# Kernel optimization log

Hardware: AMD Instinct MI355X
Metric: run time of the kernel (lower is better)

Reference implementation:

```python
import jax, jax.numpy as jnp
import numpy as np
import math

B, L, D, H = 2, 2048, 1024, 16
DK = D // H  # 64


def _lin(k, din, dout):
    kw, kb = jax.random.split(k)
    w = jax.random.normal(kw, (din, dout), dtype=jnp.float32) * 0.02
    b = jax.random.normal(kb, (dout,), dtype=jnp.float32) * 0.02
    return w, b


def setup_inputs() -> dict:
    key = jax.random.key(0)
    ks = jax.random.split(key, 12)
    wq, bq = _lin(ks[0], D, D)
    wk, bk = _lin(ks[1], D, D)
    wv, bv = _lin(ks[2], D, D)
    wo, bo = _lin(ks[3], D, D)
    whq, bhq = _lin(ks[4], DK, DK)
    whk, bhk = _lin(ks[5], DK, DK)
    whv, bhv = _lin(ks[6], DK, DK)
    who, bho = _lin(ks[7], DK, DK)
    return {
        "q_input": jax.random.normal(ks[8], (B, L, D), dtype=jnp.float32),
        "k_input": jax.random.normal(ks[9], (B, L, D), dtype=jnp.float32),
        "v_input": jax.random.normal(ks[10], (B, L, D), dtype=jnp.float32),
        "mask": jnp.ones((B, 1, L, L), dtype=jnp.int32),
        "wq": wq, "bq": bq, "wk": wk, "bk": bk, "wv": wv, "bv": bv,
        "wo": wo, "bo": bo,
        "whq": whq, "bhq": bhq, "whk": whk, "bhk": bhk,
        "whv": whv, "bhv": bhv, "who": who, "bho": bho,
    }


def reference(q_input, k_input, v_input, mask, wq, bq, wk, bk, wv, bv, wo, bo,
              whq, bhq, whk, bhk, whv, bhv, who, bho):
    scale = 1.0 / math.sqrt(DK)
    # Q/K/V projections -> [B, H, L, DK]
    Q = (q_input @ wq + bq).reshape(B, L, H, DK).transpose(0, 2, 1, 3)
    K = (k_input @ wk + bk).reshape(B, L, H, DK).transpose(0, 2, 1, 3)
    V = (v_input @ wv + bv).reshape(B, L, H, DK).transpose(0, 2, 1, 3)
    scores = jnp.einsum('bhqd,bhkd->bhqk', Q, K) * scale  # [B,H,L,L]
    neg = jnp.finfo(scores.dtype).min
    scores = jnp.where(mask == 0, neg, scores)
    probs = jax.nn.softmax(scores, axis=-1)  # dropout is identity in eval
    attn = jnp.einsum('bhqk,bhkd->bhqd', probs, V)
    heads = attn.transpose(0, 2, 1, 3)  # [B, L, H, DK]
    # Inter-head attention over the head dimension (size H) per position
    Qh = heads @ whq + bhq
    Kh = heads @ whk + bhk
    Vh = heads @ whv + bhv
    inter = jnp.einsum('blhd,blgd->blhg', Qh, Kh) * scale  # [B,L,H,H]
    iprobs = jax.nn.softmax(inter, axis=-1)
    mixed = jnp.einsum('blhg,blgd->blhd', iprobs, Vh)  # [B,L,H,DK]
    # note: inter_head_out is defined but unused in the original forward
    concat = mixed.reshape(B, L, D)
    return concat @ wo + bo
```

## Files before the change

### kernel.cpp

```cpp
#include <hip/hip_runtime.h>
#include <hip/hip_bf16.h>

typedef __bf16 bf16_t;
typedef __bf16 bf16x4 __attribute__((ext_vector_type(4)));
typedef __bf16 bf16x8 __attribute__((ext_vector_type(8)));
typedef float f32x4 __attribute__((ext_vector_type(4)));

typedef __attribute__((address_space(1))) unsigned char glob_u8;
typedef __attribute__((address_space(3))) unsigned char lds_u8;

__device__ __forceinline__ void load_lds16(const void* g, void* l) {
    __builtin_amdgcn_global_load_lds((glob_u8*)g, (lds_u8*)l, 16, 0, 0);
}

__global__ void prep1_kernel(const int* __restrict__ mask, int* __restrict__ flags,
                             const float* __restrict__ wq, const float* __restrict__ wk,
                             const float* __restrict__ wv, bf16_t* __restrict__ wqkvT)
{
    const int bid = blockIdx.x, t = threadIdx.x;
    if (bid < 2048) {
        int b = bid >> 10, qt = (bid >> 5) & 31, kt = bid & 31;
        int ok = 1;
#pragma unroll
        for (int i = 0; i < 16; i++) {
            int e = t + i * 256; int r = e >> 6, c = e & 63;
            ok &= (mask[((size_t)b * 2048 + qt * 64 + r) * 2048 + kt * 64 + c] != 0) ? 1 : 0;
        }
        ok = __syncthreads_and(ok);
        if (t == 0) flags[bid] = ok;
    } else {
        __shared__ bf16_t tile[64][65];
        int idx = bid - 2048;
        int z = idx >> 8, rem = idx & 255;
        const float* src = (z == 0) ? wq : (z == 1) ? wk : wv;
        bf16_t* dst = wqkvT + (size_t)z * 1048576;
        int rB = (rem >> 4) * 64, cB = (rem & 15) * 64;
#pragma unroll
        for (int i = 0; i < 16; i++) {
            int e = t + i * 256; int r = e >> 6, c = e & 63;
            tile[r][c] = (bf16_t)src[(size_t)(rB + r) * 1024 + cB + c];
        }
        __syncthreads();
#pragma unroll
        for (int i = 0; i < 16; i++) {
            int e = t + i * 256; int r = e >> 6, c = e & 63;
            dst[(size_t)(cB + r) * 1024 + rB + c] = tile[c][r];
        }
    }
}

__global__ void prep2_kernel(const float* __restrict__ wo, bf16_t* __restrict__ woT,
                             const float* __restrict__ s0, const float* __restrict__ s1,
                             const float* __restrict__ s2,
                             bf16_t* __restrict__ d0, bf16_t* __restrict__ d1, bf16_t* __restrict__ d2)
{
    const int bid = blockIdx.x, t = threadIdx.x;
    if (bid < 256) {
        __shared__ bf16_t tile[64][65];
        int rB = (bid >> 4) * 64, cB = (bid & 15) * 64;
#pragma unroll
        for (int i = 0; i < 16; i++) {
            int e = t + i * 256; int r = e >> 6, c = e & 63;
            tile[r][c] = (bf16_t)wo[(size_t)(rB + r) * 1024 + cB + c];
        }
        __syncthreads();
#pragma unroll
        for (int i = 0; i < 16; i++) {
            int e = t + i * 256; int r = e >> 6, c = e & 63;
            woT[(size_t)(cB + r) * 1024 + rB + c] = tile[c][r];
        }
    } else {
        int z = bid - 256;
        const float* src = (z == 0) ? s0 : (z == 1) ? s1 : s2;
        bf16_t* dst = (z == 0) ? d0 : (z == 1) ? d1 : d2;
#pragma unroll
        for (int i = 0; i < 16; i++) {
            int e = t + i * 256; int r = e >> 6, c = e & 63;
            dst[c * 64 + r] = (bf16_t)src[r * 64 + c];
        }
    }
}

__global__ __launch_bounds__(256, 2) void gemm_qkv_kernel(
    const float* __restrict__ Aq, const float* __restrict__ Ak, const float* __restrict__ Av,
    const bf16_t* __restrict__ WT,
    const float* __restrict__ bq, const float* __restrict__ bk, const float* __restrict__ bv,
    bf16_t* __restrict__ outbase)
{
    __shared__ float  Asf[2][128 * 32];
    __shared__ bf16_t Bs[2][128 * 32];
    const int z = blockIdx.z;
    const float* A    = (z == 0) ? Aq : (z == 1) ? Ak : Av;
    const bf16_t* Bt  = WT + (size_t)z * 1048576;
    const float* bia  = (z == 0) ? bq : (z == 1) ? bk : bv;
    bf16_t* out = outbase + (size_t)z * 4194304;

    const int t = threadIdx.x;
    const int w = t >> 6, lane = t & 63;
    const int lane15 = lane & 15, quad = lane >> 4;
    const int wr = w >> 1, wc = w & 1;
    const int rowBase = blockIdx.x * 128, colBase = blockIdx.y * 128;

    const int arow = lane >> 3;
    const int achk = (lane & 7) ^ arow;
    const int brow = lane >> 2;
    const int bchk = (lane & 3) ^ ((brow >> 1) & 3);

    const float*  aspA[4];
#pragma unroll
    for (int d = 0; d < 4; d++)
        aspA[d] = A + (size_t)(rowBase + w * 32 + d * 8 + arow) * 1024 + achk * 4;
    const bf16_t* aspB[2];
#pragma unroll
    for (int d = 0; d < 2; d++)
        aspB[d] = Bt + (size_t)(colBase + w * 32 + d * 16 + brow) * 1024 + bchk * 8;

    f32x4 acc[4][4];
    f32x4 zf = {0.f, 0.f, 0.f, 0.f};
#pragma unroll
    for (int i = 0; i < 4; i++)
#pragma unroll
        for (int j = 0; j < 4; j++) acc[i][j] = zf;

    const int m7 = lane15 & 7;
    const int m3b = (lane15 >> 1) & 3;

#pragma unroll
    for (int d = 0; d < 4; d++)
        load_lds16(aspA[d], (char*)Asf[0] + (w * 32 + d * 8) * 128);
#pragma unroll
    for (int d = 0; d < 2; d++)
        load_lds16(aspB[d], (char*)Bs[0] + (w * 32 + d * 16) * 64);
    __syncthreads();

    for (int kt = 0; kt < 32; kt++) {
        const int cur = kt & 1, nxt = cur ^ 1;
        if (kt < 31) {
            const int k0 = (kt + 1) * 32;
#pragma unroll
            for (int d = 0; d < 4; d++)
                load_lds16(aspA[d] + k0, (char*)Asf[nxt] + (w * 32 + d * 8) * 128);
#pragma unroll
            for (int d = 0; d < 2; d++)
                load_lds16(aspB[d] + k0, (char*)Bs[nxt] + (w * 32 + d * 16) * 64);
        }

        bf16x8 afr[4], bfr[4];
#pragma unroll
        for (int mi = 0; mi < 4; mi++) {
            int row = wr * 64 + mi * 16 + lane15;
            int p0 = (quad * 2) ^ m7, p1 = (quad * 2 + 1) ^ m7;
            f32x4 u = *(const f32x4*)(Asf[cur] + row * 32 + p0 * 4);
            f32x4 v = *(const f32x4*)(Asf[cur] + row * 32 + p1 * 4);
            bf16x8 af;
            af[0] = (bf16_t)u[0]; af[1] = (bf16_t)u[1];
            af[2] = (bf16_t)u[2]; af[3] = (bf16_t)u[3];
            af[4] = (bf16_t)v[0]; af[5] = (bf16_t)v[1];
            af[6] = (bf16_t)v[2]; af[7] = (bf16_t)v[3];
            afr[mi] = af;
        }
#pragma unroll
        for (int ni = 0; ni < 4; ni++) {
            int row = wc * 64 + ni * 16 + lane15;
            int p = quad ^ m3b;
            bfr[ni] = *(const bf16x8*)(Bs[cur] + row * 32 + p * 8);
        }
#pragma unroll
        for (int mi = 0; mi < 4; mi++)
#pragma unroll
            for (int ni = 0; ni < 4; ni++)
                acc[mi][ni] = __builtin_amdgcn_mfma_f32_16x16x32_bf16(afr[mi], bfr[ni], acc[mi][ni], 0, 0, 0);

        __syncthreads();
    }

#pragma unroll
    for (int ni = 0; ni < 4; ni++) {
        int col = colBase + wc * 64 + ni * 16 + lane15;
        float bias = bia[col];
        int h = col >> 6, dk = col & 63;
#pragma unroll
        for (int mi = 0; mi < 4; mi++) {
#pragma unroll
            for (int r = 0; r < 4; r++) {
                int row = rowBase + wr * 64 + mi * 16 + quad * 4 + r;
                int b = row >> 11, l = row & 2047;
                float v = acc[mi][ni][r] + bias;
                size_t dst = (z < 2) ? ((((size_t)(b * 16 + h)) * 2048 + l) * 64 + dk)
                                     : ((((size_t)(b * 16 + h)) * 64 + dk) * 2048 + l);
                out[dst] = (bf16_t)v;
            }
        }
    }
}

__global__ __launch_bounds__(256, 2) void gemm_out_kernel(
    const bf16_t* __restrict__ A, const bf16_t* __restrict__ Bt,
    const float* __restrict__ bia, float* __restrict__ out)
{
    __shared__ bf16_t As[128 * 32];
    __shared__ bf16_t Bs[64 * 32];
    const int t = threadIdx.x;
    const int w = t >> 6, lane = t & 63;
    const int lane15 = lane & 15, quad = lane >> 4;
    const int wr = w >> 1, wc = w & 1;
    const int rowBase = blockIdx.x * 128, colBase = blockIdx.y * 64;

    const int brow = lane >> 2, bcol = (lane & 3) * 8;

    f32x4 acc[4][2];
    f32x4 zf = {0.f, 0.f, 0.f, 0.f};
#pragma unroll
    for (int i = 0; i < 4; i++)
#pragma unroll
        for (int j = 0; j < 2; j++) acc[i][j] = zf;

    for (int k0 = 0; k0 < 1024; k0 += 32) {
#pragma unroll
        for (int j = 0; j < 2; j++) {
            int chunk = w * 2 + j;
            load_lds16(A + (size_t)(rowBase + chunk * 16 + brow) * 1024 + k0 + bcol,
                       (char*)As + chunk * 1024);
        }
        {
            int chunk = w;
            load_lds16(Bt + (size_t)(colBase + chunk * 16 + brow) * 1024 + k0 + bcol,
                       (char*)Bs + chunk * 1024);
        }
        __syncthreads();
        bf16x8 afr[4], bfr[2];
#pragma unroll
        for (int mi = 0; mi < 4; mi++)
            afr[mi] = *(const bf16x8*)(As + (wr * 64 + mi * 16 + lane15) * 32 + quad * 8);
#pragma unroll
        for (int ni = 0; ni < 2; ni++)
            bfr[ni] = *(const bf16x8*)(Bs + (wc * 32 + ni * 16 + lane15) * 32 + quad * 8);
#pragma unroll
        for (int mi = 0; mi < 4; mi++)
#pragma unroll
            for (int ni = 0; ni < 2; ni++)
                acc[mi][ni] = __builtin_amdgcn_mfma_f32_16x16x32_bf16(afr[mi], bfr[ni], acc[mi][ni], 0, 0, 0);
        __syncthreads();
    }

#pragma unroll
    for (int ni = 0; ni < 2; ni++) {
        int col = colBase + wc * 32 + ni * 16 + lane15;
        float bias = bia[col];
#pragma unroll
        for (int mi = 0; mi < 4; mi++) {
#pragma unroll
            for (int r = 0; r < 4; r++) {
                int row = rowBase + wr * 64 + mi * 16 + quad * 4 + r;
                out[(size_t)row * 1024 + col] = acc[mi][ni][r] + bias;
            }
        }
    }
}

#define FS 72

__global__ __launch_bounds__(256, 2) void flash_kernel(
    const bf16_t* __restrict__ QKV, const int* __restrict__ mask,
    const int* __restrict__ flags, bf16_t* __restrict__ attnout)
{
    __shared__ bf16_t Ks[2][64 * FS];
    __shared__ bf16_t Vs[2][64 * FS];
    __shared__ bf16_t Ps[8 * 16 * FS];
    const int t = threadIdx.x, w = t >> 6, lane = t & 63;
    const int lane15 = lane & 15, quad = lane >> 4;
    const int qt = blockIdx.y, bh = blockIdx.x;
    const int b = bh >> 4, h = bh & 15;
    const bf16_t* Q  = QKV;
    const bf16_t* K  = QKV + 4194304;
    const bf16_t* Vt = QKV + 8388608;
    const int qrow0 = qt * 128 + w * 32;

    bf16x8 aq[2][2];
#pragma unroll
    for (int qf = 0; qf < 2; qf++) {
        const bf16_t* qb = Q + ((size_t)bh * 2048 + qrow0 + qf * 16 + lane15) * 64;
        aq[qf][0] = *(const bf16x8*)(qb + quad * 8);
        aq[qf][1] = *(const bf16x8*)(qb + 32 + quad * 8);
#pragma unroll
        for (int j = 0; j < 8; j++) {
            aq[qf][0][j] = (bf16_t)((float)aq[qf][0][j] * 0.125f);
            aq[qf][1][j] = (bf16_t)((float)aq[qf][1][j] * 0.125f);
        }
    }

    f32x4 zf = {0.f, 0.f, 0.f, 0.f};
    f32x4 o[2][4];
#pragma unroll
    for (int qf = 0; qf < 2; qf++)
#pragma unroll
        for (int df = 0; df < 4; df++) o[qf][df] = zf;
    f32x4 lsum[2] = {zf, zf};
    bf16_t* Pw0 = Ps + (w * 2 + 0) * 16 * FS;
    bf16_t* Pw1 = Ps + (w * 2 + 1) * 16 * FS;
    bf16x8 ones;
#pragma unroll
    for (int j = 0; j < 8; j++) ones[j] = (bf16_t)1.0f;

    const int e0 = t * 8, e1 = (256 + t) * 8;
    const int kr0 = e0 >> 6, kc0 = e0 & 63, kr1 = e1 >> 6, kc1 = e1 & 63;
    const int* flagrow = flags + (b * 32 + qt) * 32;
    const bf16_t* Kb  = K  + (size_t)bh * 131072;
    const bf16_t* Vtb = Vt + (size_t)bh * 131072;

    {
        bf16x8 k0v = *(const bf16x8*)(Kb  + (size_t)kr0 * 64 + kc0);
        bf16x8 k1v = *(const bf16x8*)(Kb  + (size_t)kr1 * 64 + kc1);
        bf16x8 v0v = *(const bf16x8*)(Vtb + (size_t)kr0 * 2048 + kc0);
        bf16x8 v1v = *(const bf16x8*)(Vtb + (size_t)kr1 * 2048 + kc1);
        *(bf16x8*)(Ks[0] + kr0 * FS + kc0) = k0v;
        *(bf16x8*)(Ks[0] + kr1 * FS + kc1) = k1v;
        *(bf16x8*)(Vs[0] + kr0 * FS + kc0) = v0v;
        *(bf16x8*)(Vs[0] + kr1 * FS + kc1) = v1v;
    }
    __syncthreads();

    for (int kt = 0; kt < 32; kt++) {
        const int cur = kt & 1, nxt = cur ^ 1;
        bf16x8 k0v, k1v, v0v, v1v;
        if (kt + 1 < 32) {
            int kn = (kt + 1) * 64;
            k0v = *(const bf16x8*)(Kb  + (size_t)(kn + kr0) * 64 + kc0);
            k1v = *(const bf16x8*)(Kb  + (size_t)(kn + kr1) * 64 + kc1);
            v0v = *(const bf16x8*)(Vtb + (size_t)kr0 * 2048 + kn + kc0);
            v1v = *(const bf16x8*)(Vtb + (size_t)kr1 * 2048 + kn + kc1);
        }

        f32x4 st[2][4];
#pragma unroll
        for (int kf = 0; kf < 4; kf++) {
            bf16x8 kb0 = *(const bf16x8*)(Ks[cur] + (kf * 16 + lane15) * FS + quad * 8);
            bf16x8 kb1 = *(const bf16x8*)(Ks[cur] + (kf * 16 + lane15) * FS + 32 + quad * 8);
#pragma unroll
            for (int qf = 0; qf < 2; qf++) {
                f32x4 a = zf;
                a = __builtin_amdgcn_mfma_f32_16x16x32_bf16(kb0, aq[qf][0], a, 0, 0, 0);
                a = __builtin_amdgcn_mfma_f32_16x16x32_bf16(kb1, aq[qf][1], a, 0, 0, 0);
                st[qf][kf] = a * 1.44269504f;
            }
        }
        if (kt + 1 < 32) {
            *(bf16x8*)(Ks[nxt] + kr0 * FS + kc0) = k0v;
            *(bf16x8*)(Ks[nxt] + kr1 * FS + kc1) = k1v;
            *(bf16x8*)(Vs[nxt] + kr0 * FS + kc0) = v0v;
            *(bf16x8*)(Vs[nxt] + kr1 * FS + kc1) = v1v;
        }
        if (!flagrow[kt]) {
#pragma unroll
            for (int qf = 0; qf < 2; qf++)
#pragma unroll
                for (int kf = 0; kf < 4; kf++)
#pragma unroll
                    for (int r = 0; r < 4; r++) {
                        int qrow = qrow0 + qf * 16 + lane15;
                        int kpos = kt * 64 + kf * 16 + quad * 4 + r;
                        if (mask[((size_t)b * 2048 + qrow) * 2048 + kpos] == 0)
                            st[qf][kf][r] = -1e30f;
                    }
        }
#pragma unroll
        for (int qf = 0; qf < 2; qf++) {
            bf16_t* Pq = qf ? Pw1 : Pw0;
#pragma unroll
            for (int kf = 0; kf < 4; kf++) {
                bf16x4 pv;
#pragma unroll
                for (int r = 0; r < 4; r++) pv[r] = (bf16_t)exp2f(st[qf][kf][r]);
                *(bf16x4*)(Pq + lane15 * FS + kf * 16 + quad * 4) = pv;
            }
        }
        bf16x8 pa[2][2];
        pa[0][0] = *(const bf16x8*)(Pw0 + lane15 * FS + quad * 8);
        pa[0][1] = *(const bf16x8*)(Pw0 + lane15 * FS + 32 + quad * 8);
        pa[1][0] = *(const bf16x8*)(Pw1 + lane15 * FS + quad * 8);
        pa[1][1] = *(const bf16x8*)(Pw1 + lane15 * FS + 32 + quad * 8);
#pragma unroll
        for (int qf = 0; qf < 2; qf++) {
            lsum[qf] = __builtin_amdgcn_mfma_f32_16x16x32_bf16(ones, pa[qf][0], lsum[qf], 0, 0, 0);
            lsum[qf] = __builtin_amdgcn_mfma_f32_16x16x32_bf16(ones, pa[qf][1], lsum[qf], 0, 0, 0);
        }
#pragma unroll
        for (int df = 0; df < 4; df++) {
            bf16x8 vb0 = *(const bf16x8*)(Vs[cur] + (df * 16 + lane15) * FS + quad * 8);
            bf16x8 vb1 = *(const bf16x8*)(Vs[cur] + (df * 16 + lane15) * FS + 32 + quad * 8);
#pragma unroll
            for (int qf = 0; qf < 2; qf++) {
                o[qf][df] = __builtin_amdgcn_mfma_f32_16x16x32_bf16(pa[qf][0], vb0, o[qf][df], 0, 0, 0);
                o[qf][df] = __builtin_amdgcn_mfma_f32_16x16x32_bf16(pa[qf][1], vb1, o[qf][df], 0, 0, 0);
            }
        }
        __syncthreads();
    }

#pragma unroll
    for (int qf = 0; qf < 2; qf++) {
        float lv = lsum[qf][0];
#pragma unroll
        for (int r = 0; r < 4; r++) {
            float inv = 1.0f / __shfl(lv, quad * 4 + r, 64);
            size_t row = (size_t)b * 2048 + qrow0 + qf * 16 + quad * 4 + r;
#pragma unroll
            for (int df = 0; df < 4; df++)
                attnout[(row * 16 + h) * 64 + df * 16 + lane15] = (bf16_t)(o[qf][df][r] * inv);
        }
    }
}

__global__ __launch_bounds__(256, 2) void interhead_kernel(
    const bf16_t* __restrict__ attn,
    const bf16_t* __restrict__ whqT, const float* __restrict__ bhq,
    const bf16_t* __restrict__ whkT, const float* __restrict__ bhk,
    const bf16_t* __restrict__ whvT, const float* __restrict__ bhv,
    bf16_t* __restrict__ concat)
{
    __shared__ bf16_t lds[4 * 4608];
    const int t = threadIdx.x, w = t >> 6, lane = t & 63;
    const int lane15 = lane & 15, quad = lane >> 4;
    bf16_t* Qh  = lds + w * 4608;
    bf16_t* Kh  = Qh + 1024;
    bf16_t* VhT = Kh + 1024;
    bf16_t* P16 = VhT + 2048;
    const int p = blockIdx.x * 4 + w;

    bf16x8 z8 = {(bf16_t)0.f, (bf16_t)0.f, (bf16_t)0.f, (bf16_t)0.f,
                 (bf16_t)0.f, (bf16_t)0.f, (bf16_t)0.f, (bf16_t)0.f};
    ((bf16x8*)P16)[lane] = z8;
#pragma unroll
    for (int i = 0; i < 4; i++) ((bf16x8*)VhT)[i * 64 + lane] = z8;

    const bf16_t* hb = attn + ((size_t)p * 16 + lane15) * 64;
    bf16x8 ha0 = *(const bf16x8*)(hb + quad * 8);
    bf16x8 ha1 = *(const bf16x8*)(hb + 32 + quad * 8);

    const bf16_t* Wt[3] = {whqT, whkT, whvT};
    const float*  Bb[3] = {bhq, bhk, bhv};
    f32x4 zf = {0.f, 0.f, 0.f, 0.f};
#pragma unroll
    for (int m3 = 0; m3 < 3; m3++) {
#pragma unroll
        for (int nf = 0; nf < 4; nf++) {
            f32x4 acc = zf;
            bf16x8 wb0 = *(const bf16x8*)(Wt[m3] + (nf * 16 + lane15) * 64 + quad * 8);
            bf16x8 wb1 = *(const bf16x8*)(Wt[m3] + (nf * 16 + lane15) * 64 + 32 + quad * 8);
            acc = __builtin_amdgcn_mfma_f32_16x16x32_bf16(ha0, wb0, acc, 0, 0, 0);
            acc = __builtin_amdgcn_mfma_f32_16x16x32_bf16(ha1, wb1, acc, 0, 0, 0);
            float bias = Bb[m3][nf * 16 + lane15];
#pragma unroll
            for (int r = 0; r < 4; r++) {
                float v = acc[r] + bias;
                if (m3 == 0) v *= 0.125f;
                if (m3 == 2) VhT[(nf * 16 + lane15) * 32 + quad * 4 + r] = (bf16_t)v;
                else if (m3 == 0) Qh[(quad * 4 + r) * 64 + nf * 16 + lane15] = (bf16_t)v;
                else Kh[(quad * 4 + r) * 64 + nf * 16 + lane15] = (bf16_t)v;
            }
        }
    }
    __syncthreads();

    bf16x8 qa0 = *(const bf16x8*)(Qh + lane15 * 64 + quad * 8);
    bf16x8 qa1 = *(const bf16x8*)(Qh + lane15 * 64 + 32 + quad * 8);
    bf16x8 kb0 = *(const bf16x8*)(Kh + lane15 * 64 + quad * 8);
    bf16x8 kb1 = *(const bf16x8*)(Kh + lane15 * 64 + 32 + quad * 8);
    f32x4 s = zf;
    s = __builtin_amdgcn_mfma_f32_16x16x32_bf16(qa0, kb0, s, 0, 0, 0);
    s = __builtin_amdgcn_mfma_f32_16x16x32_bf16(qa1, kb1, s, 0, 0, 0);
#pragma unroll
    for (int r = 0; r < 4; r++) {
        float v = s[r];
        float mx = v;
        mx = fmaxf(mx, __shfl_xor(mx, 1));
        mx = fmaxf(mx, __shfl_xor(mx, 2));
        mx = fmaxf(mx, __shfl_xor(mx, 4));
        mx = fmaxf(mx, __shfl_xor(mx, 8));
        float pv = __expf(v - mx);
        float sm = pv;
        sm += __shfl_xor(sm, 1);
        sm += __shfl_xor(sm, 2);
        sm += __shfl_xor(sm, 4);
        sm += __shfl_xor(sm, 8);
        P16[(quad * 4 + r) * 32 + lane15] = (bf16_t)(pv / sm);
    }
    __syncthreads();

    bf16x8 pa = *(const bf16x8*)(P16 + lane15 * 32 + quad * 8);
    bf16_t* outp = concat + (size_t)p * 1024;
#pragma unroll
    for (int df = 0; df < 4; df++) {
        bf16x8 vb = *(const bf16x8*)(VhT + (df * 16 + lane15) * 32 + quad * 8);
        f32x4 mix = zf;
        mix = __builtin_amdgcn_mfma_f32_16x16x32_bf16(pa, vb, mix, 0, 0, 0);
#pragma unroll
        for (int r = 0; r < 4; r++)
            outp[(quad * 4 + r) * 64 + df * 16 + lane15] = (bf16_t)mix[r];
    }
}

extern "C" void kernel_launch(void* const* d_in, const int* in_sizes, int n_in,
                              void* d_out, int out_size, void* d_ws, size_t ws_size,
                              hipStream_t stream)
{
    const float* q_in = (const float*)d_in[0];
    const float* k_in = (const float*)d_in[1];
    const float* v_in = (const float*)d_in[2];
    const int*   mask = (const int*)d_in[3];
    const float* wq = (const float*)d_in[4];
    const float* bq = (const float*)d_in[5];
    const float* wk = (const float*)d_in[6];
    const float* bk = (const float*)d_in[7];
    const float* wv = (const float*)d_in[8];
    const float* bv = (const float*)d_in[9];
    const float* wo = (const float*)d_in[10];
    const float* bo = (const float*)d_in[11];
    const float* whq = (const float*)d_in[12];
    const float* bhq = (const float*)d_in[13];
    const float* whk = (const float*)d_in[14];
    const float* bhk = (const float*)d_in[15];
    const float* whv = (const float*)d_in[16];
    const float* bhv = (const float*)d_in[17];
    float* out = (float*)d_out;

    char* ws = (char*)d_ws;
    bf16_t* qkvb  = (bf16_t*)ws;
    bf16_t* concat = qkvb;
    bf16_t* woT   = (bf16_t*)(ws + 8u * 1024 * 1024);
    bf16_t* whqT  = (bf16_t*)(ws + 10u * 1024 * 1024);
    bf16_t* whkT  = whqT + 4096;
    bf16_t* whvT  = whqT + 8192;
    bf16_t* attnb = (bf16_t*)d_out;
    bf16_t* wqkvT = (bf16_t*)((char*)d_out + 8u * 1024 * 1024);
    int*    flags = (int*)((char*)d_out + 14u * 1024 * 1024);

    prep1_kernel<<<2816, 256, 0, stream>>>(mask, flags, wq, wk, wv, wqkvT);
    gemm_qkv_kernel<<<dim3(32, 8, 3), 256, 0, stream>>>(q_in, k_in, v_in, wqkvT, bq, bk, bv, qkvb);
    flash_kernel<<<dim3(32, 16), 256, 0, stream>>>(qkvb, mask, flags, attnb);
    prep2_kernel<<<259, 256, 0, stream>>>(wo, woT, whq, whk, whv, whqT, whkT, whvT);
    interhead_kernel<<<1024, 256, 0, stream>>>(attnb, whqT, bhq, whkT, bhk, whvT, bhv, concat);
    gemm_out_kernel<<<dim3(32, 16), 256, 0, stream>>>(concat, woT, bo, out);
    (void)in_sizes; (void)n_in; (void)out_size; (void)ws_size;
}
```

Baseline: 318.5 us.

## Triple-buffer QKV GEMM LDS tiles with prefetch distance two and partial vmcnt waits

After: 329.2 us. +3.4%, slower.

```diff
diff --git a/kernel.cpp b/kernel.cpp
--- a/kernel.cpp
+++ b/kernel.cpp
@@ -87,8 +87,8 @@
     const float* __restrict__ bq, const float* __restrict__ bk, const float* __restrict__ bv,
     bf16_t* __restrict__ outbase)
 {
-    __shared__ float  Asf[2][128 * 32];
-    __shared__ bf16_t Bs[2][128 * 32];
+    __shared__ float  Asf[3][128 * 32];
+    __shared__ bf16_t Bs[3][128 * 32];
     const int z = blockIdx.z;
     const float* A    = (z == 0) ? Aq : (z == 1) ? Ak : Av;
     const bf16_t* Bt  = WT + (size_t)z * 1048576;
@@ -131,18 +131,30 @@
 #pragma unroll
     for (int d = 0; d < 2; d++)
         load_lds16(aspB[d], (char*)Bs[0] + (w * 32 + d * 16) * 64);
-    __syncthreads();
+#pragma unroll
+    for (int d = 0; d < 4; d++)
+        load_lds16(aspA[d] + 32, (char*)Asf[1] + (w * 32 + d * 8) * 128);
+#pragma unroll
+    for (int d = 0; d < 2; d++)
+        load_lds16(aspB[d] + 32, (char*)Bs[1] + (w * 32 + d * 16) * 64);
+    asm volatile("s_waitcnt vmcnt(6)" ::: "memory");
+    __builtin_amdgcn_s_barrier();
+    __builtin_amdgcn_sched_barrier(0);
 
     for (int kt = 0; kt < 32; kt++) {
-        const int cur = kt & 1, nxt = cur ^ 1;
-        if (kt < 31) {
-            const int k0 = (kt + 1) * 32;
+        const int cur = kt % 3;
+        const float*  Ac = Asf[0] + cur * (128 * 32);
+        const bf16_t* Bc = Bs[0]  + cur * (128 * 32);
+
+        if (kt < 30) {
+            const int pre = (kt + 2) % 3;
+            const int k0 = (kt + 2) * 32;
 #pragma unroll
             for (int d = 0; d < 4; d++)
-                load_lds16(aspA[d] + k0, (char*)Asf[nxt] + (w * 32 + d * 8) * 128);
+                load_lds16(aspA[d] + k0, (char*)Asf[0] + pre * 16384 + (w * 32 + d * 8) * 128);
 #pragma unroll
             for (int d = 0; d < 2; d++)
-                load_lds16(aspB[d] + k0, (char*)Bs[nxt] + (w * 32 + d * 16) * 64);
+                load_lds16(aspB[d] + k0, (char*)Bs[0] + pre * 8192 + (w * 32 + d * 16) * 64);
         }
 
         bf16x8 afr[4], bfr[4];
@@ -150,8 +162,8 @@
         for (int mi = 0; mi < 4; mi++) {
             int row = wr * 64 + mi * 16 + lane15;
             int p0 = (quad * 2) ^ m7, p1 = (quad * 2 + 1) ^ m7;
-            f32x4 u = *(const f32x4*)(Asf[cur] + row * 32 + p0 * 4);
-            f32x4 v = *(const f32x4*)(Asf[cur] + row * 32 + p1 * 4);
+            f32x4 u = *(const f32x4*)(Ac + row * 32 + p0 * 4);
+            f32x4 v = *(const f32x4*)(Ac + row * 32 + p1 * 4);
             bf16x8 af;
             af[0] = (bf16_t)u[0]; af[1] = (bf16_t)u[1];
             af[2] = (bf16_t)u[2]; af[3] = (bf16_t)u[3];
@@ -163,7 +175,7 @@
         for (int ni = 0; ni < 4; ni++) {
             int row = wc * 64 + ni * 16 + lane15;
             int p = quad ^ m3b;
-            bfr[ni] = *(const bf16x8*)(Bs[cur] + row * 32 + p * 8);
+            bfr[ni] = *(const bf16x8*)(Bc + row * 32 + p * 8);
         }
 #pragma unroll
         for (int mi = 0; mi < 4; mi++)
@@ -171,7 +183,12 @@
             for (int ni = 0; ni < 4; ni++)
                 acc[mi][ni] = __builtin_amdgcn_mfma_f32_16x16x32_bf16(afr[mi], bfr[ni], acc[mi][ni], 0, 0, 0);
 
-        __syncthreads();
+        if (kt < 31) {
+            if (kt < 30) asm volatile("s_waitcnt vmcnt(6)" ::: "memory");
+            else         asm volatile("s_waitcnt vmcnt(0)" ::: "memory");
+            __builtin_amdgcn_s_barrier();
+            __builtin_amdgcn_sched_barrier(0);
+        }
     }
 
 #pragma unroll
```
